# Kernel optimization log

Measured on AMD Instinct MI355X. Metric: run time of the kernel, lower is better.

Reference implementation:

```python
import jax, jax.numpy as jnp
import numpy as np

H, W = 2048, 2048
N_PTS = 1_000_000
N_POS = 100_000
EMB = 32

def setup_inputs() -> dict:
    key = jax.random.key(0)
    ks = jax.random.split(key, 12)
    scale = jnp.array([H, W], dtype=jnp.float32)
    x = jax.random.uniform(ks[0], (N_PTS, 2), dtype=jnp.float32) * (scale - 1.0)
    positions = jax.random.uniform(ks[1], (N_POS, 2), dtype=jnp.float32) * scale
    neighbor_map = jax.random.randint(ks[2], (H, W, 4), 0, N_POS, dtype=jnp.int32)
    embeddings = jax.random.normal(ks[3], (N_POS, EMB), dtype=jnp.float32) * 0.001
    W1 = jax.random.normal(ks[4], (64, EMB), dtype=jnp.float32) / np.sqrt(EMB)
    b1 = jax.random.normal(ks[5], (64,), dtype=jnp.float32) * 0.01
    W2 = jax.random.normal(ks[6], (64, 64), dtype=jnp.float32) / np.sqrt(64)
    b2 = jax.random.normal(ks[7], (64,), dtype=jnp.float32) * 0.01
    W3 = jax.random.normal(ks[8], (3, 64), dtype=jnp.float32) / np.sqrt(64)
    b3 = jax.random.normal(ks[9], (3,), dtype=jnp.float32) * 0.01
    mu = jax.random.uniform(ks[10], (3,), dtype=jnp.float32)
    std = jax.random.uniform(ks[11], (3,), dtype=jnp.float32) + 0.1
    return {"x": x, "positions": positions, "neighbor_map": neighbor_map,
            "embeddings": embeddings, "W1": W1, "b1": b1, "W2": W2, "b2": b2,
            "W3": W3, "b3": b3, "mu": mu, "std": std}

def reference(x, positions, neighbor_map, embeddings, W1, b1, W2, b2, W3, b3, mu, std):
    # LatentMap: floor -> neighbor gather -> distance-weighted embedding sum
    int_pos = jnp.floor(x).astype(jnp.int32)                 # [N, 2]
    nb = neighbor_map[int_pos[:, 0], int_pos[:, 1]]          # [N, 4]
    nb_pos = positions[nb]                                   # [N, 4, 2]
    diff = nb_pos - int_pos[:, None, :].astype(jnp.float32)  # [N, 4, 2]
    dist = jax.lax.stop_gradient(jnp.linalg.norm(diff, axis=-1))  # [N, 4]
    latent = jnp.einsum('nk,nkd->nd', dist, embeddings[nb])  # [N, 32]
    # tiny MLP (equinox Linear: y = x @ W.T + b), relu on hidden layers
    h = jax.nn.relu(latent @ W1.T + b1)
    h = jax.nn.relu(h @ W2.T + b2)
    out = h @ W3.T + b3                                      # [N, 3]
    # denormalize (mu/std are stop_gradient'ed in the original)
    out = out * jax.lax.stop_gradient(std) + jax.lax.stop_gradient(mu)
    # NaN-guarded clip: per-point cond(any NaN -> mu, else clip to [0,1])
    has_nan = jnp.any(jnp.isnan(out), axis=-1, keepdims=True)
    return jnp.where(has_nan, jax.lax.stop_gradient(mu), jnp.clip(out, 0.0, 1.0))
```

## Files before the change

kernel.cpp:

```cpp
#include <hip/hip_runtime.h>
#include <hip/hip_bf16.h>


typedef __attribute__((ext_vector_type(2))) float f32x2;
typedef __attribute__((ext_vector_type(4))) float f32x4;
typedef __attribute__((ext_vector_type(4))) int   i32x4;
typedef __attribute__((ext_vector_type(8))) short s16x8;

#define GRID_W  2048
#define LSTR    36
#define PSTR    68
#define SEL_HI  0x05040100u
#define SEL_LO  0x07060302u
#define LGKM0   0xC07F

static __device__ __forceinline__ unsigned bits_bf2(__hip_bfloat162 h) {
    union { __hip_bfloat162 b; unsigned u; } cv; cv.b = h; return cv.u;
}
static __device__ __forceinline__ void split2_packed(float v0, float v1, unsigned &p0, unsigned &p1) {
    float2 f; f.x = v0; f.y = v1;
    unsigned hu = bits_bf2(__float22bfloat162_rn(f));
    float2 d;
    d.x = v0 - __uint_as_float(hu << 16);
    d.y = v1 - __uint_as_float(hu & 0xffff0000u);
    unsigned lu = bits_bf2(__float22bfloat162_rn(d));
    p0 = (hu & 0xffffu) | (lu << 16);
    p1 = (hu >> 16) | (lu & 0xffff0000u);
}
static __device__ __forceinline__ s16x8 unpack8(uint4 q0, uint4 q1, unsigned sel) {
    union { unsigned u[4]; s16x8 v; } r;
    r.u[0] = __builtin_amdgcn_perm(q0.y, q0.x, sel);
    r.u[1] = __builtin_amdgcn_perm(q0.w, q0.z, sel);
    r.u[2] = __builtin_amdgcn_perm(q1.y, q1.x, sel);
    r.u[3] = __builtin_amdgcn_perm(q1.w, q1.z, sel);
    return r.v;
}
static __device__ __forceinline__ s16x8 load_wbf(const float* p) {
    f32x4 a = ((const f32x4*)p)[0];
    f32x4 b = ((const f32x4*)p)[1];
    union { unsigned u[4]; s16x8 v; } r;
    float2 f;
    f.x = a.x; f.y = a.y; r.u[0] = bits_bf2(__float22bfloat162_rn(f));
    f.x = a.z; f.y = a.w; r.u[1] = bits_bf2(__float22bfloat162_rn(f));
    f.x = b.x; f.y = b.y; r.u[2] = bits_bf2(__float22bfloat162_rn(f));
    f.x = b.z; f.y = b.w; r.u[3] = bits_bf2(__float22bfloat162_rn(f));
    return r.v;
}
static __device__ __forceinline__ void lds_fence() {
    __builtin_amdgcn_wave_barrier();
    __builtin_amdgcn_s_waitcnt(LGKM0);
    __builtin_amdgcn_wave_barrier();
}

__global__ __launch_bounds__(256, 2) void fused_persistent(
    const float* __restrict__ x,
    const float* __restrict__ positions,
    const int*   __restrict__ nbmap,
    const float* __restrict__ emb,
    const float* __restrict__ W1,
    const float* __restrict__ b1,
    const float* __restrict__ W2,
    const float* __restrict__ b2,
    const float* __restrict__ W3,
    const float* __restrict__ b3,
    const float* __restrict__ mu,
    const float* __restrict__ sd,
    float* __restrict__ out,
    int npts)
{
    const int tid  = threadIdx.x;
    const int w    = tid >> 6;
    const int lid  = tid & 63;
    const int quad = lid >> 4;
    const int m16  = lid & 15;
    const int c8   = lid & 7;
    const int pr   = lid >> 3;

    const int nwav = gridDim.x * 4;
    const int wgid = blockIdx.x * 4 + w;
    const int NCH  = (npts + 31) >> 5;
    if (wgid >= NCH) return;

    __shared__ __align__(16) unsigned lat_lds[4 * 32 * LSTR];
    unsigned* latw = lat_lds + w * 32 * LSTR;
    unsigned* hb   = latw;

    const f32x2* Xv  = (const f32x2*)x;
    const f32x2* Pv  = (const f32x2*)positions;
    const i32x4* NBq = (const i32x4*)nbmap;

    s16x8 w1f[4];
#pragma unroll
    for (int nt = 0; nt < 4; ++nt)
        w1f[nt] = load_wbf(W1 + (nt * 16 + m16) * 32 + quad * 8);
    s16x8 w2f[2][4];
#pragma unroll
    for (int s = 0; s < 2; ++s)
#pragma unroll
        for (int nt = 0; nt < 4; ++nt)
            w2f[s][nt] = load_wbf(W2 + (nt * 16 + m16) * 64 + s * 32 + quad * 8);
    s16x8 w3f[2];
#pragma unroll
    for (int s = 0; s < 2; ++s) {
        if (m16 < 3) {
            w3f[s] = load_wbf(W3 + m16 * 64 + s * 32 + quad * 8);
        } else {
            s16x8 z = {0, 0, 0, 0, 0, 0, 0, 0};
            w3f[s] = z;
        }
    }
    float b1v[4], b2v[4];
#pragma unroll
    for (int nt = 0; nt < 4; ++nt) { b1v[nt] = b1[nt * 16 + m16]; b2v[nt] = b2[nt * 16 + m16]; }
    const int mm = (m16 < 3) ? m16 : 0;
    const float b3m = b3[mm], sdm = sd[mm], mum = mu[mm];

    f32x2 xv[4], xvn[4];
    i32x4 nb[4], nbn[4];
#pragma unroll
    for (int p = 0; p < 4; ++p) {
        int g = wgid * 32 + p * 8 + pr;
        g = (g < npts) ? g : (npts - 1);
        xv[p] = Xv[g];
    }
#pragma unroll
    for (int p = 0; p < 4; ++p) {
        int i0 = (int)xv[p].x, i1 = (int)xv[p].y;
        nb[p] = NBq[i0 * GRID_W + i1];
    }

    for (int c = wgid; c < NCH; c += nwav) {
        const int cn = c + nwav;
        const bool hn = (cn < NCH);

        if (hn) {
#pragma unroll
            for (int p = 0; p < 4; ++p) {
                int g = cn * 32 + p * 8 + pr;
                g = (g < npts) ? g : (npts - 1);
                xvn[p] = Xv[g];
            }
        }

#pragma unroll
        for (int p = 0; p < 4; ++p) {
            f32x2 xvp = xv[p];
            float f0 = (float)(int)xvp.x, f1 = (float)(int)xvp.y;
            i32x4 n4 = nb[p];
            int ids[4] = {n4.x, n4.y, n4.z, n4.w};
            float a0 = 0.f, a1 = 0.f, a2 = 0.f, a3 = 0.f;
#pragma unroll
            for (int k = 0; k < 4; ++k) {
                f32x2 pp = Pv[ids[k]];
                float dx = pp.x - f0, dy = pp.y - f1;
                float dist = sqrtf(dx * dx + dy * dy);
                f32x4 e = *(const f32x4*)(emb + ids[k] * 32 + c8 * 4);
                a0 = fmaf(dist, e.x, a0); a1 = fmaf(dist, e.y, a1);
                a2 = fmaf(dist, e.z, a2); a3 = fmaf(dist, e.w, a3);
            }
            unsigned p0, p1, p2, p3;
            split2_packed(a0, a1, p0, p1);
            split2_packed(a2, a3, p2, p3);
            uint4 pv; pv.x = p0; pv.y = p1; pv.z = p2; pv.w = p3;
            *(uint4*)(latw + (p * 8 + pr) * LSTR + c8 * 4) = pv;
        }
        lds_fence();

        s16x8 AH[2], AL[2];
#pragma unroll
        for (int t = 0; t < 2; ++t) {
            const unsigned* ap = latw + (t * 16 + m16) * LSTR + quad * 8;
            uint4 q0 = *(const uint4*)ap;
            uint4 q1 = *(const uint4*)(ap + 4);
            AH[t] = unpack8(q0, q1, SEL_HI);
            AL[t] = unpack8(q0, q1, SEL_LO);
        }
        lds_fence();

        if (hn) {
#pragma unroll
            for (int p = 0; p < 4; ++p) {
                int i0 = (int)xvn[p].x, i1 = (int)xvn[p].y;
                nbn[p] = NBq[i0 * GRID_W + i1];
            }
        }

#pragma unroll
        for (int t = 0; t < 2; ++t) {
            s16x8 ah = AH[t], al = AL[t];
            f32x4 c1[4];
#pragma unroll
            for (int nt = 0; nt < 4; ++nt) {
                f32x4 cc = {0.f, 0.f, 0.f, 0.f};
                cc = __builtin_amdgcn_mfma_f32_16x16x32_bf16(al, w1f[nt], cc, 0, 0, 0);
                cc = __builtin_amdgcn_mfma_f32_16x16x32_bf16(ah, w1f[nt], cc, 0, 0, 0);
                c1[nt] = cc;
            }
            __builtin_amdgcn_wave_barrier();
#pragma unroll
            for (int nt = 0; nt < 4; ++nt)
#pragma unroll
                for (int r = 0; r < 4; r += 2) {
                    float v0 = fmaxf(c1[nt][r]     + b1v[nt], 0.f);
                    float v1 = fmaxf(c1[nt][r + 1] + b1v[nt], 0.f);
                    unsigned p0, p1; split2_packed(v0, v1, p0, p1);
                    hb[(quad * 4 + r)     * PSTR + nt * 16 + m16] = p0;
                    hb[(quad * 4 + r + 1) * PSTR + nt * 16 + m16] = p1;
                }
            lds_fence();

            f32x4 c2[4] = {{0.f,0.f,0.f,0.f},{0.f,0.f,0.f,0.f},{0.f,0.f,0.f,0.f},{0.f,0.f,0.f,0.f}};
#pragma unroll
            for (int s = 0; s < 2; ++s) {
                const unsigned* rp = hb + m16 * PSTR + s * 32 + quad * 8;
                uint4 h0 = *(const uint4*)rp;
                uint4 h1 = *(const uint4*)(rp + 4);
                s16x8 a2h = unpack8(h0, h1, SEL_HI);
                s16x8 a2l = unpack8(h0, h1, SEL_LO);
#pragma unroll
                for (int nt = 0; nt < 4; ++nt) {
                    c2[nt] = __builtin_amdgcn_mfma_f32_16x16x32_bf16(a2l, w2f[s][nt], c2[nt], 0, 0, 0);
                    c2[nt] = __builtin_amdgcn_mfma_f32_16x16x32_bf16(a2h, w2f[s][nt], c2[nt], 0, 0, 0);
                }
            }
            lds_fence();
#pragma unroll
            for (int nt = 0; nt < 4; ++nt)
#pragma unroll
                for (int r = 0; r < 4; r += 2) {
                    float v0 = fmaxf(c2[nt][r]     + b2v[nt], 0.f);
                    float v1 = fmaxf(c2[nt][r + 1] + b2v[nt], 0.f);
                    unsigned p0, p1; split2_packed(v0, v1, p0, p1);
                    hb[(quad * 4 + r)     * PSTR + nt * 16 + m16] = p0;
                    hb[(quad * 4 + r + 1) * PSTR + nt * 16 + m16] = p1;
                }
            lds_fence();

            f32x4 c3 = {0.f, 0.f, 0.f, 0.f};
#pragma unroll
            for (int s = 0; s < 2; ++s) {
                const unsigned* rp = hb + m16 * PSTR + s * 32 + quad * 8;
                uint4 h0 = *(const uint4*)rp;
                uint4 h1 = *(const uint4*)(rp + 4);
                s16x8 a3h = unpack8(h0, h1, SEL_HI);
                s16x8 a3l = unpack8(h0, h1, SEL_LO);
                c3 = __builtin_amdgcn_mfma_f32_16x16x32_bf16(a3l, w3f[s], c3, 0, 0, 0);
                c3 = __builtin_amdgcn_mfma_f32_16x16x32_bf16(a3h, w3f[s], c3, 0, 0, 0);
            }
            lds_fence();
#pragma unroll
            for (int r = 0; r < 4; ++r) {
                float v = (c3[r] + b3m) * sdm + mum;
                v = fminf(fmaxf(v, 0.f), 1.f);
                int gpt = c * 32 + t * 16 + quad * 4 + r;
                if (m16 < 3 && gpt < npts) out[(size_t)gpt * 3 + m16] = v;
            }
        }

        if (hn) {
#pragma unroll
            for (int p = 0; p < 4; ++p) { xv[p] = xvn[p]; nb[p] = nbn[p]; }
        }
    }
}

extern "C" void kernel_launch(void* const* d_in, const int* in_sizes, int n_in,
                              void* d_out, int out_size, void* d_ws, size_t ws_size,
                              hipStream_t stream) {
    const float* x         = (const float*)d_in[0];
    const float* positions = (const float*)d_in[1];
    const int*   nbmap     = (const int*)d_in[2];
    const float* emb       = (const float*)d_in[3];
    const float* W1        = (const float*)d_in[4];
    const float* b1        = (const float*)d_in[5];
    const float* W2        = (const float*)d_in[6];
    const float* b2        = (const float*)d_in[7];
    const float* W3        = (const float*)d_in[8];
    const float* b3        = (const float*)d_in[9];
    const float* mu        = (const float*)d_in[10];
    const float* sd        = (const float*)d_in[11];
    float* out = (float*)d_out;

    int npts = in_sizes[0] / 2;
    int nch = (npts + 31) / 32;
    int blocks = 1024;
    int maxb = (nch + 3) / 4;
    if (blocks > maxb) blocks = maxb;
    fused_persistent<<<blocks, 256, 0, stream>>>(x, positions, nbmap, emb,
                                                 W1, b1, W2, b2, W3, b3, mu, sd,
                                                 out, npts);
}
```

Measured before the change: 223.4 us.

## Gather embeddings directly into MFMA A-fragment layout, dropping LDS latent staging

Each lane now gathers the 8 embedding values it needs for the MFMA A operand (point m16, k-slice quad*8) and splits them into bf16 hi/lo registers directly. This removes the LDS write, fence and read-back of the latent tile. In exchange each point's neighbor lookups, position loads and sqrt run on 4 lanes (one per quad) instead of being spread out, so per-lane gather work and redundant address traffic go up. LDS use shrinks to the hidden-layer buffer only.

```diff
diff --git a/kernel.cpp b/kernel.cpp
--- a/kernel.cpp
+++ b/kernel.cpp
@@ -8,7 +8,6 @@
 typedef __attribute__((ext_vector_type(8))) short s16x8;
 
 #define GRID_W  2048
-#define LSTR    36
 #define PSTR    68
 #define SEL_HI  0x05040100u
 #define SEL_LO  0x07060302u
@@ -26,6 +25,14 @@
     unsigned lu = bits_bf2(__float22bfloat162_rn(d));
     p0 = (hu & 0xffffu) | (lu << 16);
     p1 = (hu >> 16) | (lu & 0xffff0000u);
+}
+static __device__ __forceinline__ void split2_frag(float v0, float v1, unsigned &hu, unsigned &lu) {
+    float2 f; f.x = v0; f.y = v1;
+    hu = bits_bf2(__float22bfloat162_rn(f));
+    float2 d;
+    d.x = v0 - __uint_as_float(hu << 16);
+    d.y = v1 - __uint_as_float(hu & 0xffff0000u);
+    lu = bits_bf2(__float22bfloat162_rn(d));
 }
 static __device__ __forceinline__ s16x8 unpack8(uint4 q0, uint4 q1, unsigned sel) {
     union { unsigned u[4]; s16x8 v; } r;
@@ -73,17 +80,14 @@
     const int lid  = tid & 63;
     const int quad = lid >> 4;
     const int m16  = lid & 15;
-    const int c8   = lid & 7;
-    const int pr   = lid >> 3;
 
     const int nwav = gridDim.x * 4;
     const int wgid = blockIdx.x * 4 + w;
     const int NCH  = (npts + 31) >> 5;
     if (wgid >= NCH) return;
 
-    __shared__ __align__(16) unsigned lat_lds[4 * 32 * LSTR];
-    unsigned* latw = lat_lds + w * 32 * LSTR;
-    unsigned* hb   = latw;
+    __shared__ __align__(16) unsigned h_lds[4 * 16 * PSTR];
+    unsigned* hb = h_lds + w * 16 * PSTR;
 
     const f32x2* Xv  = (const f32x2*)x;
     const f32x2* Pv  = (const f32x2*)positions;
@@ -115,18 +119,18 @@
     const int mm = (m16 < 3) ? m16 : 0;
     const float b3m = b3[mm], sdm = sd[mm], mum = mu[mm];
 
-    f32x2 xv[4], xvn[4];
-    i32x4 nb[4], nbn[4];
-#pragma unroll
-    for (int p = 0; p < 4; ++p) {
-        int g = wgid * 32 + p * 8 + pr;
+    f32x2 xv[2], xvn[2];
+    i32x4 nb[2], nbn[2];
+#pragma unroll
+    for (int t = 0; t < 2; ++t) {
+        int g = wgid * 32 + t * 16 + m16;
         g = (g < npts) ? g : (npts - 1);
-        xv[p] = Xv[g];
-    }
-#pragma unroll
-    for (int p = 0; p < 4; ++p) {
-        int i0 = (int)xv[p].x, i1 = (int)xv[p].y;
-        nb[p] = NBq[i0 * GRID_W + i1];
+        xv[t] = Xv[g];
+    }
+#pragma unroll
+    for (int t = 0; t < 2; ++t) {
+        int i0 = (int)xv[t].x, i1 = (int)xv[t].y;
+        nb[t] = NBq[i0 * GRID_W + i1];
     }
 
     for (int c = wgid; c < NCH; c += nwav) {
@@ -135,53 +139,48 @@
 
         if (hn) {
 #pragma unroll
-            for (int p = 0; p < 4; ++p) {
-                int g = cn * 32 + p * 8 + pr;
+            for (int t = 0; t < 2; ++t) {
+                int g = cn * 32 + t * 16 + m16;
                 g = (g < npts) ? g : (npts - 1);
-                xvn[p] = Xv[g];
-            }
-        }
-
-#pragma unroll
-        for (int p = 0; p < 4; ++p) {
-            f32x2 xvp = xv[p];
+                xvn[t] = Xv[g];
+            }
+        }
+
+        s16x8 AH[2], AL[2];
+#pragma unroll
+        for (int t = 0; t < 2; ++t) {
+            f32x2 xvp = xv[t];
             float f0 = (float)(int)xvp.x, f1 = (float)(int)xvp.y;
-            i32x4 n4 = nb[p];
+            i32x4 n4 = nb[t];
             int ids[4] = {n4.x, n4.y, n4.z, n4.w};
             float a0 = 0.f, a1 = 0.f, a2 = 0.f, a3 = 0.f;
+            float a4 = 0.f, a5 = 0.f, a6 = 0.f, a7 = 0.f;
 #pragma unroll
             for (int k = 0; k < 4; ++k) {
                 f32x2 pp = Pv[ids[k]];
                 float dx = pp.x - f0, dy = pp.y - f1;
                 float dist = sqrtf(dx * dx + dy * dy);
-                f32x4 e = *(const f32x4*)(emb + ids[k] * 32 + c8 * 4);
-                a0 = fmaf(dist, e.x, a0); a1 = fmaf(dist, e.y, a1);
-                a2 = fmaf(dist, e.z, a2); a3 = fmaf(dist, e.w, a3);
-            }
-            unsigned p0, p1, p2, p3;
-            split2_packed(a0, a1, p0, p1);
-            split2_packed(a2, a3, p2, p3);
-            uint4 pv; pv.x = p0; pv.y = p1; pv.z = p2; pv.w = p3;
-            *(uint4*)(latw + (p * 8 + pr) * LSTR + c8 * 4) = pv;
-        }
-        lds_fence();
-
-        s16x8 AH[2], AL[2];
-#pragma unroll
-        for (int t = 0; t < 2; ++t) {
-            const unsigned* ap = latw + (t * 16 + m16) * LSTR + quad * 8;
-            uint4 q0 = *(const uint4*)ap;
-            uint4 q1 = *(const uint4*)(ap + 4);
-            AH[t] = unpack8(q0, q1, SEL_HI);
-            AL[t] = unpack8(q0, q1, SEL_LO);
-        }
-        lds_fence();
+                const f32x4* ep = (const f32x4*)(emb + ids[k] * 32 + quad * 8);
+                f32x4 e0 = ep[0];
+                f32x4 e1 = ep[1];
+                a0 = fmaf(dist, e0.x, a0); a1 = fmaf(dist, e0.y, a1);
+                a2 = fmaf(dist, e0.z, a2); a3 = fmaf(dist, e0.w, a3);
+                a4 = fmaf(dist, e1.x, a4); a5 = fmaf(dist, e1.y, a5);
+                a6 = fmaf(dist, e1.z, a6); a7 = fmaf(dist, e1.w, a7);
+            }
+            union { unsigned u[4]; s16x8 v; } rh, rl;
+            split2_frag(a0, a1, rh.u[0], rl.u[0]);
+            split2_frag(a2, a3, rh.u[1], rl.u[1]);
+            split2_frag(a4, a5, rh.u[2], rl.u[2]);
+            split2_frag(a6, a7, rh.u[3], rl.u[3]);
+            AH[t] = rh.v; AL[t] = rl.v;
+        }
 
         if (hn) {
 #pragma unroll
-            for (int p = 0; p < 4; ++p) {
-                int i0 = (int)xvn[p].x, i1 = (int)xvn[p].y;
-                nbn[p] = NBq[i0 * GRID_W + i1];
+            for (int t = 0; t < 2; ++t) {
+                int i0 = (int)xvn[t].x, i1 = (int)xvn[t].y;
+                nbn[t] = NBq[i0 * GRID_W + i1];
             }
         }
 
@@ -259,7 +258,7 @@
 
         if (hn) {
 #pragma unroll
-            for (int p = 0; p < 4; ++p) { xv[p] = xvn[p]; nb[p] = nbn[p]; }
+            for (int t = 0; t < 2; ++t) { xv[t] = xvn[t]; nb[t] = nbn[t]; }
         }
     }
 }
```

Measured after the change: 229.7 us. 2.8% more time.
